# Kernel tuning notes

Measured on AMD Instinct MI355X. Metric: run time of the kernel, lower is better.

The kernel has to match this reference:

```python
import jax, jax.numpy as jnp
import numpy as np

B = 2; N_RAW = 16384; N_KP = 2048; M_VOX = 8192; C_VOX = 64
H_BEV, W_BEV, C_BEV, BEV_STRIDE = 200, 176, 256, 8
VOXEL_SIZE = np.array([0.05, 0.05, 0.1], np.float32)
PC_MIN = np.array([0.0, -40.0, -3.0], np.float32)
DOWNSAMPLE = 4
RAW_RADII = (0.4, 0.8); RAW_NS = (16, 16)
CONV_RADII = (1.2, 2.4); CONV_NS = (16, 32)
BN_SCALE = float(1.0 / np.sqrt(1.0 + 1e-5))  # eval-mode BN, running mean=0 var=1


def _fps_idx(pts, n):
    # farthest point sampling over pts [N,3] -> [n] int32 indices
    N = pts.shape[0]
    def step(carry, _):
        dists, last = carry
        d = jnp.sum((pts - pts[last]) ** 2, axis=-1)
        dists = jnp.minimum(dists, d)
        nxt = jnp.argmax(dists).astype(jnp.int32)
        return (dists, nxt), nxt
    init = (jnp.full((N,), 1e10, pts.dtype), jnp.int32(0))
    _, rest = jax.lax.scan(step, init, None, length=n - 1)
    return jnp.concatenate([jnp.zeros((1,), jnp.int32), rest])


def _bilinear(bev, x, y):
    # bev [H,W,C]; faithful to bilinear_interpolate_bev (clamp then weight)
    H, W, _ = bev.shape
    xf = jnp.floor(x); yf = jnp.floor(y)
    x0 = jnp.clip(xf.astype(jnp.int32), 0, W - 1)
    x1 = jnp.clip(xf.astype(jnp.int32) + 1, 0, W - 1)
    y0 = jnp.clip(yf.astype(jnp.int32), 0, H - 1)
    y1 = jnp.clip(yf.astype(jnp.int32) + 1, 0, H - 1)
    fa = bev[y1, x0]; fb = bev[y1, x1]; fc = bev[y0, x1]; fd = bev[y0, x0]
    x0f = x0.astype(x.dtype); x1f = x1.astype(x.dtype)
    y0f = y0.astype(y.dtype); y1f = y1.astype(y.dtype)
    wa = (x - x0f) * (y1f - y); wb = (x1f - x) * (y1f - y)
    wc = (x1f - x) * (y - y0f); wd = (x - x0f) * (y - y0f)
    return fd * wb[:, None] + fc * wa[:, None] + fa * wc[:, None] + fb * wd[:, None]


def _group(xyz, feats, new_xyz, radius, nsample):
    # ball query: first nsample points within radius (original order), pad with first hit
    M = xyz.shape[0]
    d2 = jnp.sum((new_xyz[:, None, :] - xyz[None, :, :]) ** 2, axis=-1)  # [K,M]
    mask = d2 < radius * radius
    key = jnp.where(mask, jnp.arange(M, dtype=jnp.int32)[None, :], M)
    idx = jnp.sort(key, axis=1)[:, :nsample]
    empty = ~jnp.any(mask, axis=1)
    idx = jnp.where(idx < M, idx, idx[:, :1])
    idx = jnp.clip(idx, 0, M - 1)
    g_xyz = xyz[idx] - new_xyz[:, None, :]
    g = jnp.concatenate([g_xyz, feats[idx]], axis=-1)  # [K,ns,3+C]
    return jnp.where(empty[:, None, None], 0.0, g), empty


def _bn_relu(x, g, b):
    return jax.nn.relu(x * (g * BN_SCALE) + b)


def _sa(xyz, feats, new_xyz, radii, nss, w0, g0, b0, w1, g1, b1):
    outs = []
    for i, (r, ns) in enumerate(zip(radii, nss)):
        grouped, empty = jax.vmap(lambda x, f, nx: _group(x, f, nx, r, ns))(xyz, feats, new_xyz)
        h = _bn_relu(grouped @ w0[i], g0[i], b0[i])
        h = _bn_relu(h @ w1[i], g1[i], b1[i])
        pooled = jnp.max(h, axis=2)  # [B,K,Cout]
        outs.append(jnp.where(empty[..., None], 0.0, pooled))
    return jnp.concatenate(outs, axis=-1)


def _forward(points, spatial_features, voxel_coords, voxel_features,
             raw_w0, raw_g0, raw_b0, raw_w1, raw_g1, raw_b1,
             conv_w0, conv_g0, conv_b0, conv_w1, conv_g1, conv_b1,
             fusion_w, fusion_g, fusion_b):
    pts = points.reshape(B, N_RAW, -1)
    xyz_raw = pts[..., 1:4]
    idxs = jax.vmap(lambda p: _fps_idx(p, N_KP))(jax.lax.stop_gradient(xyz_raw))
    kp = jnp.take_along_axis(xyz_raw, idxs[..., None], axis=1)  # [B,NKP,3]
    xi = (kp[..., 0] - PC_MIN[0]) / VOXEL_SIZE[0] / BEV_STRIDE
    yi = (kp[..., 1] - PC_MIN[1]) / VOXEL_SIZE[1] / BEV_STRIDE
    bev = jnp.transpose(spatial_features, (0, 2, 3, 1))  # [B,H,W,C]
    bev_feat = jax.vmap(_bilinear)(bev, xi, yi)  # [B,NKP,C_BEV]
    raw_feat = _sa(xyz_raw, pts[..., 4:], kp, RAW_RADII, RAW_NS,
                   raw_w0, raw_g0, raw_b0, raw_w1, raw_g1, raw_b1)
    vc = voxel_coords.reshape(B, M_VOX, 4)
    centers = (vc[..., jnp.array([3, 2, 1])].astype(jnp.float32) + 0.5) \
        * jnp.asarray(VOXEL_SIZE * DOWNSAMPLE) + jnp.asarray(PC_MIN)
    conv_feat = _sa(centers, voxel_features.reshape(B, M_VOX, C_VOX), kp, CONV_RADII, CONV_NS,
                    conv_w0, conv_g0, conv_b0, conv_w1, conv_g1, conv_b1)
    feats = jnp.concatenate([bev_feat, raw_feat, conv_feat], axis=-1).reshape(B * N_KP, -1)
    return _bn_relu(feats @ fusion_w, fusion_g, fusion_b)  # [B*NKP, 128]


def setup_inputs():
    key = jax.random.key(0)
    ks = jax.random.split(key, 8)
    xyz = jax.random.uniform(ks[0], (B * N_RAW, 3), jnp.float32) * jnp.array([70.4, 80.0, 4.0]) + jnp.array([0.0, -40.0, -3.0])
    inten = jax.random.uniform(ks[1], (B * N_RAW, 1), jnp.float32)
    bidx = jnp.repeat(jnp.arange(B, dtype=jnp.float32), N_RAW)[:, None]
    points = jnp.concatenate([bidx, xyz, inten], axis=1)
    spatial_features = jax.random.normal(ks[2], (B, C_BEV, H_BEV, W_BEV), jnp.float32)
    vb = jnp.repeat(jnp.arange(B, dtype=jnp.int32), M_VOX)[:, None]
    vz = jax.random.randint(ks[3], (B * M_VOX, 1), 0, 10, jnp.int32)
    vy = jax.random.randint(ks[4], (B * M_VOX, 1), 0, 400, jnp.int32)
    vx = jax.random.randint(ks[5], (B * M_VOX, 1), 0, 352, jnp.int32)
    voxel_coords = jnp.concatenate([vb, vz, vy, vx], axis=1)
    voxel_features = jax.random.normal(ks[6], (B * M_VOX, C_VOX), jnp.float32)
    pk = jax.random.split(ks[7], 5)
    w = lambda k, s: jax.random.normal(k, s, jnp.float32) * 0.05
    return dict(
        points=points, spatial_features=spatial_features,
        voxel_coords=voxel_coords, voxel_features=voxel_features,
        raw_w0=w(pk[0], (2, 4, 16)), raw_g0=jnp.ones((2, 16)), raw_b0=jnp.zeros((2, 16)),
        raw_w1=w(pk[1], (2, 16, 16)), raw_g1=jnp.ones((2, 16)), raw_b1=jnp.zeros((2, 16)),
        conv_w0=w(pk[2], (2, 67, 64)), conv_g0=jnp.ones((2, 64)), conv_b0=jnp.zeros((2, 64)),
        conv_w1=w(pk[3], (2, 64, 64)), conv_g1=jnp.ones((2, 64)), conv_b1=jnp.zeros((2, 64)),
        fusion_w=w(pk[4], (416, 128)), fusion_g=jnp.ones((128,)), fusion_b=jnp.zeros((128,)))


def reference(points, spatial_features, voxel_coords, voxel_features,
              raw_w0, raw_g0, raw_b0, raw_w1, raw_g1, raw_b1,
              conv_w0, conv_g0, conv_b0, conv_w1, conv_g1, conv_b1,
              fusion_w, fusion_g, fusion_b):
    return _forward(points, spatial_features, voxel_coords, voxel_features,
                    raw_w0, raw_g0, raw_b0, raw_w1, raw_g1, raw_b1,
                    conv_w0, conv_g0, conv_b0, conv_w1, conv_g1, conv_b1,
                    fusion_w, fusion_g, fusion_b)
```

## Files before the change

### kernel.cpp

```cpp
#include <hip/hip_runtime.h>


#define NRAW   16384
#define MVOX   8192
#define NKP    2048
#define NKPALL 4096

__device__ __constant__ float kBNS = (float)0.9999950000374997;

__global__ __launch_bounds__(256) void prep_kernel(
    const float* __restrict__ pts, const int* __restrict__ vc,
    float4* __restrict__ xyz4, float4* __restrict__ cxyz4) {
#pragma clang fp contract(off)
  int i = blockIdx.x * 256 + threadIdx.x;
  if (i < 2 * NRAW) {
    const float* p = pts + (size_t)i * 5;
    xyz4[i] = make_float4(p[1], p[2], p[3], p[4]);
  }
  if (i < 2 * MVOX) {
    const int* v = vc + (size_t)i * 4;
    cxyz4[i] = make_float4(((float)v[3] + 0.5f) * 0.2f + 0.0f,
                           ((float)v[2] + 0.5f) * 0.2f + -40.0f,
                           ((float)v[1] + 0.5f) * 0.4f + -3.0f, 0.f);
  }
}

__global__ __launch_bounds__(1024) void sort_kernel(
    const float* __restrict__ pts, int* __restrict__ sperm) {
  const int b = blockIdx.x, t = threadIdx.x;
  __shared__ unsigned hist[256], cur[256];
  if (t < 256) hist[t] = 0u;
  __syncthreads();
  int bins[16];
#pragma unroll
  for (int k = 0; k < 16; ++k) {
    const int i = k * 1024 + t;
    const float y = pts[(size_t)(b * NRAW + i) * 5 + 2];
    int bin = (int)((y + 40.0f) * 3.2f);
    bin = bin < 0 ? 0 : (bin > 255 ? 255 : bin);
    bins[k] = bin;
    atomicAdd(&hist[bin], 1u);
  }
  __syncthreads();
  if (t == 0) {
    unsigned acc = 0;
    for (int i = 0; i < 256; ++i) { cur[i] = acc; acc += hist[i]; }
  }
  __syncthreads();
#pragma unroll
  for (int k = 0; k < 16; ++k) {
    const int i = k * 1024 + t;
    const unsigned pos = atomicAdd(&cur[bins[k]], 1u);
    sperm[b * NRAW + pos] = i;
  }
}

__device__ __forceinline__ unsigned wave_umax63(unsigned v) {
  unsigned t;
  t = (unsigned)__builtin_amdgcn_update_dpp(0, (int)v, 0xB1,  0xf, 0xf, true); v = v < t ? t : v;
  t = (unsigned)__builtin_amdgcn_update_dpp(0, (int)v, 0x4E,  0xf, 0xf, true); v = v < t ? t : v;
  t = (unsigned)__builtin_amdgcn_update_dpp(0, (int)v, 0x124, 0xf, 0xf, true); v = v < t ? t : v;
  t = (unsigned)__builtin_amdgcn_update_dpp(0, (int)v, 0x128, 0xf, 0xf, true); v = v < t ? t : v;
  t = (unsigned)__builtin_amdgcn_update_dpp(0, (int)v, 0x142, 0xa, 0xf, true); v = v < t ? t : v;
  t = (unsigned)__builtin_amdgcn_update_dpp(0, (int)v, 0x143, 0xc, 0xf, true); v = v < t ? t : v;
  return v;
}

__global__ __launch_bounds__(1024, 4) void fps_kernel(
    const int* __restrict__ sperm, const float4* __restrict__ xyz4,
    float* __restrict__ kx, float* __restrict__ ky, float* __restrict__ kz) {
#pragma clang fp contract(off)
  const int b = blockIdx.x;
  const int t = threadIdx.x;
  const int w = t >> 6, lane = t & 63;
  const int wb = w * 1024;
  const int base = b * NRAW;

  __shared__ unsigned long long slot[3];

  int pj[16];
  float px[16], py[16], pz[16], dd[16];
#pragma unroll
  for (int j = 0; j < 16; ++j)
    pj[j] = sperm[base + wb + j * 64 + lane];
#pragma unroll
  for (int j = 0; j < 16; ++j) {
    const float4 q = xyz4[base + pj[j]];
    px[j] = q.x; py[j] = q.y; pz[j] = q.z; dd[j] = 1e10f;
  }
  if (t < 3) slot[t] = 0ULL;

  float bnx = px[0], bxx = px[0], bny = py[0], bxy = py[0], bnz = pz[0], bxz = pz[0];
#pragma unroll
  for (int j = 1; j < 16; ++j) {
    bnx = fminf(bnx, px[j]); bxx = fmaxf(bxx, px[j]);
    bny = fminf(bny, py[j]); bxy = fmaxf(bxy, py[j]);
    bnz = fminf(bnz, pz[j]); bxz = fmaxf(bxz, pz[j]);
  }
#pragma unroll
  for (int off = 1; off < 64; off <<= 1) {
    bnx = fminf(bnx, __shfl_xor(bnx, off, 64));
    bxx = fmaxf(bxx, __shfl_xor(bxx, off, 64));
    bny = fminf(bny, __shfl_xor(bny, off, 64));
    bxy = fmaxf(bxy, __shfl_xor(bxy, off, 64));
    bnz = fminf(bnz, __shfl_xor(bnz, off, 64));
    bxz = fmaxf(bxz, __shfl_xor(bxz, off, 64));
  }

  const float4 p0 = xyz4[base];
  float lx = p0.x, ly = p0.y, lz = p0.z;
  if (t == 0) { kx[b * NKP] = lx; ky[b * NKP] = ly; kz[b * NKP] = lz; }

  unsigned long long cpk = 0ULL;
  float bvc = __builtin_inff();
  __syncthreads();

  for (int s = 1; s < NKP; ++s) {
    float dxm = fmaxf(fmaxf(bnx - lx, lx - bxx), 0.f);
    float dym = fmaxf(fmaxf(bny - ly, ly - bxy), 0.f);
    float dzm = fmaxf(fmaxf(bnz - lz, lz - bxz), 0.f);
    const float LB2 = dxm * dxm + dym * dym + dzm * dzm;
    if (!(LB2 * 0.9999f > bvc)) {
#pragma unroll
      for (int j = 0; j < 16; ++j) {
        float dx = px[j] - lx, dy = py[j] - ly, dz = pz[j] - lz;
        float d2 = dx * dx; d2 = d2 + dy * dy; d2 = d2 + dz * dz;
        dd[j] = fminf(dd[j], d2);
      }
      float m8[8];
#pragma unroll
      for (int j = 0; j < 8; ++j) m8[j] = fmaxf(dd[2 * j], dd[2 * j + 1]);
      float m4[4];
#pragma unroll
      for (int j = 0; j < 4; ++j) m4[j] = fmaxf(m8[2 * j], m8[2 * j + 1]);
      const float bv = fmaxf(fmaxf(m4[0], m4[1]), fmaxf(m4[2], m4[3]));

      const unsigned vb = __float_as_uint(bv);
      const unsigned wmax =
          (unsigned)__builtin_amdgcn_readlane((int)wave_umax63(vb), 63);
      unsigned mo = 0xFFFFFFFFu;
      if (vb == wmax) {
#pragma unroll
        for (int j = 0; j < 16; ++j)
          if (__float_as_uint(dd[j]) == wmax) {
            const unsigned o = (unsigned)pj[j];
            mo = o < mo ? o : mo;
          }
      }
      const unsigned cand = (vb == wmax) ? ~mo : 0u;
      const unsigned cm =
          (unsigned)__builtin_amdgcn_readlane((int)wave_umax63(cand), 63);
      cpk = ((unsigned long long)wmax << 32) | (unsigned long long)cm;
      bvc = __uint_as_float(wmax);
    }
    if (lane == 63) atomicMax(&slot[s % 3], cpk);
    __syncthreads();

    const unsigned long long g = slot[s % 3];
    const int wi = __builtin_amdgcn_readfirstlane((int)~(unsigned)g);
    if (t == 0) slot[(s + 2) % 3] = 0ULL;
    const float4 cw = xyz4[base + wi];
    lx = cw.x; ly = cw.y; lz = cw.z;
    if (t == 0) { kx[b * NKP + s] = lx; ky[b * NKP + s] = ly; kz[b * NKP + s] = lz; }
  }
}

__global__ __launch_bounds__(256) void bev_kernel(
    const float* __restrict__ sf, const float* __restrict__ kx,
    const float* __restrict__ ky, float* __restrict__ feats) {
#pragma clang fp contract(off)
  const int kidx = blockIdx.x;
  const int c = threadIdx.x;
  const int b = kidx >> 11;
  const float x = (kx[kidx] - 0.0f) / 0.05f / 8.0f;
  const float y = (ky[kidx] - (-40.0f)) / 0.05f / 8.0f;
  const float xf = floorf(x), yf = floorf(y);
  int x0 = (int)xf;     x0 = x0 < 0 ? 0 : (x0 > 175 ? 175 : x0);
  int x1 = (int)xf + 1; x1 = x1 < 0 ? 0 : (x1 > 175 ? 175 : x1);
  int y0 = (int)yf;     y0 = y0 < 0 ? 0 : (y0 > 199 ? 199 : y0);
  int y1 = (int)yf + 1; y1 = y1 < 0 ? 0 : (y1 > 199 ? 199 : y1);
  const float x0f = (float)x0, x1f = (float)x1, y0f = (float)y0, y1f = (float)y1;
  const float wa = (x - x0f) * (y1f - y);
  const float wb = (x1f - x) * (y1f - y);
  const float wc = (x1f - x) * (y - y0f);
  const float wd = (x - x0f) * (y - y0f);
  const float* base = sf + ((size_t)b * 256 + c) * (200 * 176);
  const float fa = base[y1 * 176 + x0];
  const float fb = base[y1 * 176 + x1];
  const float fc = base[y0 * 176 + x1];
  const float fd = base[y0 * 176 + x0];
  float r = fd * wb; r = r + fc * wa; r = r + fa * wc; r = r + fb * wd;
  feats[(size_t)kidx * 416 + c] = r;
}

__global__ __launch_bounds__(256) void raw_sa_kernel(
    const float4* __restrict__ xyz4,
    const float* __restrict__ kx, const float* __restrict__ ky,
    const float* __restrict__ kz,
    const float* __restrict__ w0, const float* __restrict__ g0,
    const float* __restrict__ b0, const float* __restrict__ w1,
    const float* __restrict__ g1, const float* __restrict__ b1,
    float* __restrict__ feats) {
  const int wv = threadIdx.x >> 6;
  const int lane = threadIdx.x & 63;
  const int gw = blockIdx.x * 4 + wv;
  const int ri = gw >> 12;
  const int kidx = gw & 4095;
  const int b = kidx >> 11;
  const float R2 = ri ? (float)(0.8 * 0.8) : (float)(0.4 * 0.4);

  __shared__ int   idxl[4][16];
  __shared__ float hbuf[4][16][17];

  const float kxv = kx[kidx], kyv = ky[kidx], kzv = kz[kidx];
  const int base = b * NRAW;
  int cnt = 0;
  {
#pragma clang fp contract(off)
    for (int ch = 0; ch < NRAW / 64 && cnt < 16; ++ch) {
      const float4 q = xyz4[base + ch * 64 + lane];
      float dx = kxv - q.x, dy = kyv - q.y, dz = kzv - q.z;
      float d2 = dx * dx; d2 = d2 + dy * dy; d2 = d2 + dz * dz;
      unsigned long long m = __ballot(d2 < R2);
      while (m && cnt < 16) {
        int bit = __builtin_ctzll(m);
        if (lane == 0) idxl[wv][cnt] = ch * 64 + bit;
        ++cnt;
        m &= m - 1;
      }
    }
  }
  const int outoff = kidx * 416 + 256 + ri * 16;
  if (cnt == 0) {
    if (lane < 16) feats[outoff + lane] = 0.f;
    return;
  }
  __threadfence_block();

  const int s = lane & 15, cq = lane >> 4;
  const int ss = (s < cnt) ? s : 0;
  const float4 q = xyz4[base + idxl[wv][ss]];
  const float gx = q.x - kxv, gy = q.y - kyv, gz = q.z - kzv, gi = q.w;
  const int wb0 = ri * 64, cb = ri * 16;
#pragma unroll
  for (int j = 0; j < 4; ++j) {
    int c = cq * 4 + j;
    float a = gx * w0[wb0 + c];
    a = fmaf(gy, w0[wb0 + 16 + c], a);
    a = fmaf(gz, w0[wb0 + 32 + c], a);
    a = fmaf(gi, w0[wb0 + 48 + c], a);
    a = fmaf(a, g0[cb + c] * kBNS, b0[cb + c]);
    hbuf[wv][s][c] = fmaxf(a, 0.f);
  }
  __threadfence_block();
  float o0 = 0.f, o1 = 0.f, o2 = 0.f, o3 = 0.f;
  const int wb1 = ri * 256;
#pragma unroll
  for (int k = 0; k < 16; ++k) {
    float hk = hbuf[wv][s][k];
    o0 = fmaf(hk, w1[wb1 + k * 16 + cq * 4 + 0], o0);
    o1 = fmaf(hk, w1[wb1 + k * 16 + cq * 4 + 1], o1);
    o2 = fmaf(hk, w1[wb1 + k * 16 + cq * 4 + 2], o2);
    o3 = fmaf(hk, w1[wb1 + k * 16 + cq * 4 + 3], o3);
  }
  float v0 = fmaxf(fmaf(o0, g1[cb + cq * 4 + 0] * kBNS, b1[cb + cq * 4 + 0]), 0.f);
  float v1 = fmaxf(fmaf(o1, g1[cb + cq * 4 + 1] * kBNS, b1[cb + cq * 4 + 1]), 0.f);
  float v2 = fmaxf(fmaf(o2, g1[cb + cq * 4 + 2] * kBNS, b1[cb + cq * 4 + 2]), 0.f);
  float v3 = fmaxf(fmaf(o3, g1[cb + cq * 4 + 3] * kBNS, b1[cb + cq * 4 + 3]), 0.f);
#pragma unroll
  for (int off = 1; off < 16; off <<= 1) {
    v0 = fmaxf(v0, __shfl_xor(v0, off, 64));
    v1 = fmaxf(v1, __shfl_xor(v1, off, 64));
    v2 = fmaxf(v2, __shfl_xor(v2, off, 64));
    v3 = fmaxf(v3, __shfl_xor(v3, off, 64));
  }
  if (s == 0) {
    feats[outoff + cq * 4 + 0] = v0;
    feats[outoff + cq * 4 + 1] = v1;
    feats[outoff + cq * 4 + 2] = v2;
    feats[outoff + cq * 4 + 3] = v3;
  }
}

__global__ __launch_bounds__(256) void conv_sa_kernel(
    const float4* __restrict__ cxyz4, const float* __restrict__ vf,
    const float* __restrict__ kx, const float* __restrict__ ky,
    const float* __restrict__ kz,
    const float* __restrict__ w0, const float* __restrict__ g0,
    const float* __restrict__ b0, const float* __restrict__ w1,
    const float* __restrict__ g1, const float* __restrict__ b1,
    float* __restrict__ feats) {
  const int wv = threadIdx.x >> 6;
  const int lane = threadIdx.x & 63;
  const int gw = blockIdx.x * 4 + wv;
  const int ri = gw >> 12;
  const int kidx = gw & 4095;
  const int b = kidx >> 11;
  const int NS = ri ? 32 : 16;
  const float R2 = ri ? (float)(2.4 * 2.4) : (float)(1.2 * 1.2);

  __shared__ int   idxl[4][32];
  __shared__ float gbuf[4][64];
  __shared__ float hbuf[4][32][64];

  const float kxv = kx[kidx], kyv = ky[kidx], kzv = kz[kidx];
  const int base = b * MVOX;
  int cnt = 0;
  {
#pragma clang fp contract(off)
    for (int ch = 0; ch < MVOX / 64 && cnt < NS; ++ch) {
      const float4 q = cxyz4[base + ch * 64 + lane];
      float dx = kxv - q.x, dy = kyv - q.y, dz = kzv - q.z;
      float d2 = dx * dx; d2 = d2 + dy * dy; d2 = d2 + dz * dz;
      unsigned long long m = __ballot(d2 < R2);
      while (m && cnt < NS) {
        int bit = __builtin_ctzll(m);
        if (lane == 0) idxl[wv][cnt] = ch * 64 + bit;
        ++cnt;
        m &= m - 1;
      }
    }
  }
  const int outoff = kidx * 416 + 288 + ri * 64;
  if (cnt == 0) {
    feats[outoff + lane] = 0.f;
    return;
  }
  __threadfence_block();

  const float wA0 = w0[(ri * 67 + 0) * 64 + lane];
  const float wA1 = w0[(ri * 67 + 1) * 64 + lane];
  const float wA2 = w0[(ri * 67 + 2) * 64 + lane];
  float wB[64];
#pragma unroll
  for (int k = 0; k < 64; ++k) wB[k] = w0[(ri * 67 + 3 + k) * 64 + lane];
  float wC[64];
#pragma unroll
  for (int k = 0; k < 64; ++k) wC[k] = w1[(ri * 64 + k) * 64 + lane];
  const float s0 = g0[ri * 64 + lane] * kBNS, bb0 = b0[ri * 64 + lane];
  const float s1 = g1[ri * 64 + lane] * kBNS, bb1 = b1[ri * 64 + lane];

  for (int sm = 0; sm < cnt; ++sm) {
    const int p = base + idxl[wv][sm];
    const float4 q = cxyz4[p];
    const float ox = q.x - kxv, oy = q.y - kyv, oz = q.z - kzv;
    gbuf[wv][lane] = vf[(size_t)p * 64 + lane];
    __threadfence_block();
    float acc = ox * wA0;
    acc = fmaf(oy, wA1, acc);
    acc = fmaf(oz, wA2, acc);
#pragma unroll
    for (int k4 = 0; k4 < 16; ++k4) {
      float4 g4 = *(const float4*)&gbuf[wv][k4 * 4];
      acc = fmaf(g4.x, wB[k4 * 4 + 0], acc);
      acc = fmaf(g4.y, wB[k4 * 4 + 1], acc);
      acc = fmaf(g4.z, wB[k4 * 4 + 2], acc);
      acc = fmaf(g4.w, wB[k4 * 4 + 3], acc);
    }
    hbuf[wv][sm][lane] = fmaxf(fmaf(acc, s0, bb0), 0.f);
    __threadfence_block();
  }
  float mx = -1e30f;
  for (int sm = 0; sm < cnt; ++sm) {
    float acc = 0.f;
#pragma unroll
    for (int k4 = 0; k4 < 16; ++k4) {
      float4 h4 = *(const float4*)&hbuf[wv][sm][k4 * 4];
      acc = fmaf(h4.x, wC[k4 * 4 + 0], acc);
      acc = fmaf(h4.y, wC[k4 * 4 + 1], acc);
      acc = fmaf(h4.z, wC[k4 * 4 + 2], acc);
      acc = fmaf(h4.w, wC[k4 * 4 + 3], acc);
    }
    mx = fmaxf(mx, fmaxf(fmaf(acc, s1, bb1), 0.f));
  }
  feats[outoff + lane] = mx;
}

__global__ __launch_bounds__(256) void fusion_kernel(
    const float* __restrict__ feats, const float* __restrict__ fw,
    const float* __restrict__ fg, const float* __restrict__ fb,
    float* __restrict__ out) {
  const int gid = blockIdx.x * 256 + threadIdx.x;
  const int kidx = gid >> 7, c = gid & 127;
  const float* f = feats + (size_t)kidx * 416;
  float acc = 0.f;
#pragma unroll 4
  for (int k = 0; k < 416; k += 4) {
    float4 fv = *(const float4*)(f + k);
    acc = fmaf(fv.x, fw[(k + 0) * 128 + c], acc);
    acc = fmaf(fv.y, fw[(k + 1) * 128 + c], acc);
    acc = fmaf(fv.z, fw[(k + 2) * 128 + c], acc);
    acc = fmaf(fv.w, fw[(k + 3) * 128 + c], acc);
  }
  out[gid] = fmaxf(fmaf(acc, fg[c] * kBNS, fb[c]), 0.f);
}

extern "C" void kernel_launch(void* const* d_in, const int* in_sizes, int n_in,
                              void* d_out, int out_size, void* d_ws, size_t ws_size,
                              hipStream_t stream) {
  (void)in_sizes; (void)n_in; (void)out_size; (void)ws_size;
  const float* pts = (const float*)d_in[0];
  const float* sf  = (const float*)d_in[1];
  const int*   vc  = (const int*)d_in[2];
  const float* vf  = (const float*)d_in[3];
  const float* raw_w0 = (const float*)d_in[4];
  const float* raw_g0 = (const float*)d_in[5];
  const float* raw_b0 = (const float*)d_in[6];
  const float* raw_w1 = (const float*)d_in[7];
  const float* raw_g1 = (const float*)d_in[8];
  const float* raw_b1 = (const float*)d_in[9];
  const float* conv_w0 = (const float*)d_in[10];
  const float* conv_g0 = (const float*)d_in[11];
  const float* conv_b0 = (const float*)d_in[12];
  const float* conv_w1 = (const float*)d_in[13];
  const float* conv_g1 = (const float*)d_in[14];
  const float* conv_b1 = (const float*)d_in[15];
  const float* fus_w = (const float*)d_in[16];
  const float* fus_g = (const float*)d_in[17];
  const float* fus_b = (const float*)d_in[18];
  float* out = (float*)d_out;

  float* W = (float*)d_ws;
  float4* xyz4  = (float4*)W;
  float4* cxyz4 = (float4*)(W + 131072);
  float* kx    = W + 196608;
  float* ky    = W + 200704;
  float* kz    = W + 204800;
  float* feats = W + 208896;
  int* sperm = (int*)(W + 208896);

  prep_kernel<<<128, 256, 0, stream>>>(pts, vc, xyz4, cxyz4);
  sort_kernel<<<2, 1024, 0, stream>>>(pts, sperm);
  fps_kernel<<<2, 1024, 0, stream>>>(sperm, xyz4, kx, ky, kz);
  bev_kernel<<<NKPALL, 256, 0, stream>>>(sf, kx, ky, feats);
  raw_sa_kernel<<<2048, 256, 0, stream>>>(xyz4, kx, ky, kz,
                                          raw_w0, raw_g0, raw_b0, raw_w1, raw_g1, raw_b1,
                                          feats);
  conv_sa_kernel<<<2048, 256, 0, stream>>>(cxyz4, vf, kx, ky, kz,
                                           conv_w0, conv_g0, conv_b0, conv_w1, conv_g1, conv_b1,
                                           feats);
  fusion_kernel<<<2048, 256, 0, stream>>>(feats, fus_w, fus_g, fus_b, out);
}
```

Baseline: 2.349 ms.

## Replace FPS shared atomicMax reduction with per-wave slots and DPP cross-wave scan

The farthest-point-sampling loop no longer has each wave do an LDS atomicMax on one slot, clear a rotating slot, and then reload the winner's coordinates from global memory. Each wave's owner lane now writes a packed key plus the winner's xyz into a double-buffered per-wave LDS slot. After the barrier, every wave reads all 16 slots and reduces them with a 16-lane DPP scan, then takes the coordinates straight from LDS. This drops the atomics, the slot reset and a dependent global load from the serial per-iteration critical path, at the cost of extra LDS reads and DPP work per step, and a key packing that truncates the wave-local index to 14 bits.

```diff
diff --git a/kernel.cpp b/kernel.cpp
--- a/kernel.cpp
+++ b/kernel.cpp
@@ -66,6 +66,17 @@
   return v;
 }
 
+#define FPS_SCAN_STAGE(CTRL)                                                     \
+  {                                                                              \
+    const unsigned _lo =                                                         \
+        (unsigned)__builtin_amdgcn_update_dpp(0, (int)kl, CTRL, 0xf, 0xf, true); \
+    const unsigned _hi =                                                         \
+        (unsigned)__builtin_amdgcn_update_dpp(0, (int)kh, CTRL, 0xf, 0xf, true); \
+    const unsigned long long _t = ((unsigned long long)_hi << 32) | _lo;         \
+    const unsigned long long _c = ((unsigned long long)kh << 32) | kl;           \
+    if (_t > _c) { kl = _lo; kh = _hi; }                                         \
+  }
+
 __global__ __launch_bounds__(1024, 4) void fps_kernel(
     const int* __restrict__ sperm, const float4* __restrict__ xyz4,
     float* __restrict__ kx, float* __restrict__ ky, float* __restrict__ kz) {
@@ -76,7 +87,7 @@
   const int wb = w * 1024;
   const int base = b * NRAW;
 
-  __shared__ unsigned long long slot[3];
+  __shared__ __align__(16) unsigned slots[2][16][8];
 
   int pj[16];
   float px[16], py[16], pz[16], dd[16];
@@ -88,7 +99,6 @@
     const float4 q = xyz4[base + pj[j]];
     px[j] = q.x; py[j] = q.y; pz[j] = q.z; dd[j] = 1e10f;
   }
-  if (t < 3) slot[t] = 0ULL;
 
   float bnx = px[0], bxx = px[0], bny = py[0], bxy = py[0], bnz = pz[0], bxz = pz[0];
 #pragma unroll
@@ -111,57 +121,92 @@
   float lx = p0.x, ly = p0.y, lz = p0.z;
   if (t == 0) { kx[b * NKP] = lx; ky[b * NKP] = ly; kz[b * NKP] = lz; }
 
-  unsigned long long cpk = 0ULL;
+  unsigned c_lo = 0u, c_hi = 0u;
+  float c_x = 0.f, c_y = 0.f, c_z = 0.f;
+  bool owner = false;
   float bvc = __builtin_inff();
+
+  auto active_step = [&]() {
+#pragma clang fp contract(off)
+#pragma unroll
+    for (int j = 0; j < 16; ++j) {
+      float dx = px[j] - lx, dy = py[j] - ly, dz = pz[j] - lz;
+      float d2 = dx * dx; d2 = d2 + dy * dy; d2 = d2 + dz * dz;
+      dd[j] = fminf(dd[j], d2);
+    }
+    float m8[8];
+#pragma unroll
+    for (int j = 0; j < 8; ++j) m8[j] = fmaxf(dd[2 * j], dd[2 * j + 1]);
+    float m4[4];
+#pragma unroll
+    for (int j = 0; j < 4; ++j) m4[j] = fmaxf(m8[2 * j], m8[2 * j + 1]);
+    const float bv = fmaxf(fmaxf(m4[0], m4[1]), fmaxf(m4[2], m4[3]));
+
+    const unsigned vb = __float_as_uint(bv);
+    const unsigned wmax =
+        (unsigned)__builtin_amdgcn_readlane((int)wave_umax63(vb), 63);
+    unsigned mo = 0xFFFFFFFFu;
+    if (vb == wmax) {
+#pragma unroll
+      for (int j = 0; j < 16; ++j)
+        if (__float_as_uint(dd[j]) == wmax) {
+          const unsigned o = (unsigned)pj[j];
+          mo = o < mo ? o : mo;
+        }
+    }
+    const unsigned cand = (vb == wmax) ? ~mo : 0u;
+    const unsigned cm =
+        (unsigned)__builtin_amdgcn_readlane((int)wave_umax63(cand), 63);
+    const unsigned widx = ~cm;
+    bvc = __uint_as_float(wmax);
+    owner = (vb == wmax) && (mo == widx);
+    float ox = 0.f, oy = 0.f, oz = 0.f;
+#pragma unroll
+    for (int j = 0; j < 16; ++j) {
+      const bool h = (pj[j] == (int)widx);
+      ox = h ? px[j] : ox;
+      oy = h ? py[j] : oy;
+      oz = h ? pz[j] : oz;
+    }
+    c_x = ox; c_y = oy; c_z = oz;
+    c_lo = (wmax << 18) | ((cm & 0x3FFFu) << 4) | (unsigned)w;
+    c_hi = wmax >> 14;
+  };
+
+  active_step();
+  if (owner) {
+    *(uint4*)&slots[0][w][0] =
+        make_uint4(c_lo, c_hi, __float_as_uint(c_x), __float_as_uint(c_y));
+    slots[0][w][4] = __float_as_uint(c_z);
+  }
   __syncthreads();
 
+  const int sl = lane & 15;
   for (int s = 1; s < NKP; ++s) {
+    const int pr = (s - 1) & 1, pw = s & 1;
+    unsigned kl = slots[pr][sl][0];
+    unsigned kh = slots[pr][sl][1];
+    FPS_SCAN_STAGE(0x121)
+    FPS_SCAN_STAGE(0x122)
+    FPS_SCAN_STAGE(0x124)
+    FPS_SCAN_STAGE(0x128)
+    const int ws = (int)(kl & 0xFu);
+    lx = __uint_as_float(slots[pr][ws][2]);
+    ly = __uint_as_float(slots[pr][ws][3]);
+    lz = __uint_as_float(slots[pr][ws][4]);
+    if (t == 0) { kx[b * NKP + s] = lx; ky[b * NKP + s] = ly; kz[b * NKP + s] = lz; }
+
     float dxm = fmaxf(fmaxf(bnx - lx, lx - bxx), 0.f);
     float dym = fmaxf(fmaxf(bny - ly, ly - bxy), 0.f);
     float dzm = fmaxf(fmaxf(bnz - lz, lz - bxz), 0.f);
     const float LB2 = dxm * dxm + dym * dym + dzm * dzm;
-    if (!(LB2 * 0.9999f > bvc)) {
-#pragma unroll
-      for (int j = 0; j < 16; ++j) {
-        float dx = px[j] - lx, dy = py[j] - ly, dz = pz[j] - lz;
-        float d2 = dx * dx; d2 = d2 + dy * dy; d2 = d2 + dz * dz;
-        dd[j] = fminf(dd[j], d2);
-      }
-      float m8[8];
-#pragma unroll
-      for (int j = 0; j < 8; ++j) m8[j] = fmaxf(dd[2 * j], dd[2 * j + 1]);
-      float m4[4];
-#pragma unroll
-      for (int j = 0; j < 4; ++j) m4[j] = fmaxf(m8[2 * j], m8[2 * j + 1]);
-      const float bv = fmaxf(fmaxf(m4[0], m4[1]), fmaxf(m4[2], m4[3]));
-
-      const unsigned vb = __float_as_uint(bv);
-      const unsigned wmax =
-          (unsigned)__builtin_amdgcn_readlane((int)wave_umax63(vb), 63);
-      unsigned mo = 0xFFFFFFFFu;
-      if (vb == wmax) {
-#pragma unroll
-        for (int j = 0; j < 16; ++j)
-          if (__float_as_uint(dd[j]) == wmax) {
-            const unsigned o = (unsigned)pj[j];
-            mo = o < mo ? o : mo;
-          }
-      }
-      const unsigned cand = (vb == wmax) ? ~mo : 0u;
-      const unsigned cm =
-          (unsigned)__builtin_amdgcn_readlane((int)wave_umax63(cand), 63);
-      cpk = ((unsigned long long)wmax << 32) | (unsigned long long)cm;
-      bvc = __uint_as_float(wmax);
-    }
-    if (lane == 63) atomicMax(&slot[s % 3], cpk);
+    if (!(LB2 * 0.9999f > bvc)) active_step();
+    if (owner) {
+      *(uint4*)&slots[pw][w][0] =
+          make_uint4(c_lo, c_hi, __float_as_uint(c_x), __float_as_uint(c_y));
+      slots[pw][w][4] = __float_as_uint(c_z);
+    }
     __syncthreads();
-
-    const unsigned long long g = slot[s % 3];
-    const int wi = __builtin_amdgcn_readfirstlane((int)~(unsigned)g);
-    if (t == 0) slot[(s + 2) % 3] = 0ULL;
-    const float4 cw = xyz4[base + wi];
-    lx = cw.x; ly = cw.y; lz = cw.z;
-    if (t == 0) { kx[b * NKP + s] = lx; ky[b * NKP + s] = ly; kz[b * NKP + s] = lz; }
   }
 }
 
```

After: 3.524 ms. 50.0% more time.

## Bin FPS points into 2D x/y tiles and broadcast the winner's coordinates via LDS

Applied to the files above, without the earlier changes.

The counting sort now bins points on a 4×64 x/y grid instead of 64 y-only strips. Each wave's 1024 points therefore form a compact spatial tile, so the per-wave bounding-box lower bound skips more distance updates. Inside the FPS loop, the winning lane writes its coordinates to a double-buffered shared slot. The packed atomicMax key now carries the wave id, so after the barrier every thread reads the winner's coordinates from LDS instead of doing a dependent global load. This shortens the serial per-iteration critical path, at the cost of a few extra registers and a narrower 14-bit index field in the key.

```diff
diff --git a/kernel.cpp b/kernel.cpp
--- a/kernel.cpp
+++ b/kernel.cpp
@@ -35,9 +35,13 @@
 #pragma unroll
   for (int k = 0; k < 16; ++k) {
     const int i = k * 1024 + t;
+    const float x = pts[(size_t)(b * NRAW + i) * 5 + 1];
     const float y = pts[(size_t)(b * NRAW + i) * 5 + 2];
-    int bin = (int)((y + 40.0f) * 3.2f);
-    bin = bin < 0 ? 0 : (bin > 255 ? 255 : bin);
+    int xb = (int)(x * 0.0568181818f);
+    xb = xb < 0 ? 0 : (xb > 3 ? 3 : xb);
+    int yb = (int)((y + 40.0f) * 0.8f);
+    yb = yb < 0 ? 0 : (yb > 63 ? 63 : yb);
+    const int bin = xb * 64 + yb;
     bins[k] = bin;
     atomicAdd(&hist[bin], 1u);
   }
@@ -77,6 +81,7 @@
   const int base = b * NRAW;
 
   __shared__ unsigned long long slot[3];
+  __shared__ float4 cslot[2][16];
 
   int pj[16];
   float px[16], py[16], pz[16], dd[16];
@@ -112,9 +117,12 @@
   if (t == 0) { kx[b * NKP] = lx; ky[b * NKP] = ly; kz[b * NKP] = lz; }
 
   unsigned long long cpk = 0ULL;
+  float c_x = 0.f, c_y = 0.f, c_z = 0.f;
+  bool owner = false;
   float bvc = __builtin_inff();
   __syncthreads();
 
+  const int sl = lane & 15;
   for (int s = 1; s < NKP; ++s) {
     float dxm = fmaxf(fmaxf(bnx - lx, lx - bxx), 0.f);
     float dym = fmaxf(fmaxf(bny - ly, ly - bxy), 0.f);
@@ -139,29 +147,38 @@
       const unsigned wmax =
           (unsigned)__builtin_amdgcn_readlane((int)wave_umax63(vb), 63);
       unsigned mo = 0xFFFFFFFFu;
+      float tx = 0.f, ty = 0.f, tz = 0.f;
       if (vb == wmax) {
 #pragma unroll
         for (int j = 0; j < 16; ++j)
           if (__float_as_uint(dd[j]) == wmax) {
             const unsigned o = (unsigned)pj[j];
-            mo = o < mo ? o : mo;
+            if (o < mo) { mo = o; tx = px[j]; ty = py[j]; tz = pz[j]; }
           }
       }
       const unsigned cand = (vb == wmax) ? ~mo : 0u;
       const unsigned cm =
           (unsigned)__builtin_amdgcn_readlane((int)wave_umax63(cand), 63);
-      cpk = ((unsigned long long)wmax << 32) | (unsigned long long)cm;
+      cpk = ((unsigned long long)wmax << 32) |
+            ((unsigned long long)(cm & 0x3FFFu) << 4) | (unsigned long long)w;
       bvc = __uint_as_float(wmax);
+      owner = (cand != 0u) && (~mo == cm);
+      c_x = tx; c_y = ty; c_z = tz;
     }
     if (lane == 63) atomicMax(&slot[s % 3], cpk);
+    if (owner) cslot[s & 1][w] = make_float4(c_x, c_y, c_z, 0.f);
     __syncthreads();
 
     const unsigned long long g = slot[s % 3];
-    const int wi = __builtin_amdgcn_readfirstlane((int)~(unsigned)g);
-    if (t == 0) slot[(s + 2) % 3] = 0ULL;
-    const float4 cw = xyz4[base + wi];
-    lx = cw.x; ly = cw.y; lz = cw.z;
-    if (t == 0) { kx[b * NKP + s] = lx; ky[b * NKP + s] = ly; kz[b * NKP + s] = lz; }
+    const float4 cf = cslot[s & 1][sl];
+    const int ws = (int)((unsigned)g & 0xFu);
+    lx = __shfl(cf.x, ws, 64);
+    ly = __shfl(cf.y, ws, 64);
+    lz = __shfl(cf.z, ws, 64);
+    if (t == 0) {
+      slot[(s + 2) % 3] = 0ULL;
+      kx[b * NKP + s] = lx; ky[b * NKP + s] = ly; kz[b * NKP + s] = lz;
+    }
   }
 }
 
```

After: 3.774 ms. 60.7% more time.
